# Optimization experiments

Hardware: AMD Instinct MI355X
Metric: run time of the kernel (lower is better)

The kernel has to match this reference:

```python
import jax, jax.numpy as jnp
import numpy as np

NU, NI, E = 200000, 100000, 500000
D, H, O = 128, 256, 128  # embedding_dim, hidden_dim, output_dim


def _sage(x_src, x_dst, src, dst, n_dst, W_l, b_l, W_r):
    """PyG SAGEConv (mean aggr): lin_l(mean_j x_src[j]) + lin_r(x_dst)."""
    msgs = x_src[src]                                            # [E, d_in]
    summed = jax.ops.segment_sum(msgs, dst, num_segments=n_dst)  # [n_dst, d_in]
    deg = jax.ops.segment_sum(jnp.ones(src.shape, x_src.dtype), dst, num_segments=n_dst)
    mean = summed / jnp.maximum(deg, 1.0)[:, None]
    return mean @ W_l + b_l + x_dst @ W_r


def setup_inputs() -> dict:
    key = jax.random.key(0)
    ks = jax.random.split(key, 18)

    def w(k, i, o):
        return jax.random.normal(k, (i, o), jnp.float32) / np.float32(np.sqrt(i))

    return {
        "x_user": jax.random.normal(ks[0], (NU, D), jnp.float32),
        "x_item": jax.random.normal(ks[1], (NI, D), jnp.float32),
        "edge_src": jax.random.randint(ks[2], (E,), 0, NU, jnp.int32),
        "edge_dst": jax.random.randint(ks[3], (E,), 0, NI, jnp.int32),
        # layer 1 (encoder): D -> H, one SAGEConv per edge type
        "W_l1_ui": w(ks[4], D, H), "W_r1_ui": w(ks[5], D, H), "b_l1_ui": jnp.zeros((H,), jnp.float32),
        "W_l1_iu": w(ks[6], D, H), "W_r1_iu": w(ks[7], D, H), "b_l1_iu": jnp.zeros((H,), jnp.float32),
        # layer 2 (projection): H -> O
        "W_l2_ui": w(ks[8], H, O), "W_r2_ui": w(ks[9], H, O), "b_l2_ui": jnp.zeros((O,), jnp.float32),
        "W_l2_iu": w(ks[10], H, O), "W_r2_iu": w(ks[11], H, O), "b_l2_iu": jnp.zeros((O,), jnp.float32),
    }


def reference(x_user, x_item, edge_src, edge_dst,
              W_l1_ui, W_r1_ui, b_l1_ui, W_l1_iu, W_r1_iu, b_l1_iu,
              W_l2_ui, W_r2_ui, b_l2_ui, W_l2_iu, W_r2_iu, b_l2_iu):
    # encoder layer: relu(SAGEConv) per destination node type (dropout=eval/no-op)
    h_item = jax.nn.relu(_sage(x_user, x_item, edge_src, edge_dst, NI, W_l1_ui, b_l1_ui, W_r1_ui))
    h_user = jax.nn.relu(_sage(x_item, x_user, edge_dst, edge_src, NU, W_l1_iu, b_l1_iu, W_r1_iu))
    # extra relu in RecommendationGNN.forward is a no-op after relu
    # projection layer: relu(SAGEConv), dropout=0
    o_item = jax.nn.relu(_sage(h_user, h_item, edge_src, edge_dst, NI, W_l2_ui, b_l2_ui, W_r2_ui))
    o_user = jax.nn.relu(_sage(h_item, h_user, edge_dst, edge_src, NU, W_l2_iu, b_l2_iu, W_r2_iu))
    return (o_user, o_item)
```

## Files before the change

kernel.cpp:

```cpp
#include <hip/hip_runtime.h>
#include <stdint.h>

typedef __attribute__((ext_vector_type(8))) short short8;
typedef __attribute__((ext_vector_type(4))) float f32x4;

#define SCAN_TILE 4096

__device__ __forceinline__ float bf2f(unsigned short u) {
  union { unsigned int i; float f; } v;
  v.i = ((unsigned int)u) << 16;
  return v.f;
}
__device__ __forceinline__ unsigned short f2bf(float f) {
  union { float f; unsigned int i; } v;
  v.f = f;
  unsigned int u = v.i;
  return (unsigned short)((u + 0x7FFFu + ((u >> 16) & 1u)) >> 16);
}
__device__ __forceinline__ unsigned int pack2(float a, float b) {
  return (unsigned int)f2bf(a) | ((unsigned int)f2bf(b) << 16);
}
__device__ __forceinline__ void add2(float& a, float& b, unsigned int v) {
  a += bf2f((unsigned short)(v & 0xffff));
  b += bf2f((unsigned short)(v >> 16));
}

__device__ __forceinline__ size_t fragS128(int row, int k) {
  return ((size_t)(row >> 4) * 4 + (size_t)(k >> 5)) * 512
       + (size_t)((((row & 15) + (((k >> 3) & 3) << 4)) << 3) + (k & 7));
}

__global__ __launch_bounds__(256) void build_wt_all(
    const float* __restrict__ Wl1ui, const float* __restrict__ Wr1ui,
    const float* __restrict__ Wl1iu, const float* __restrict__ Wr1iu,
    const float* __restrict__ Wl2ui, const float* __restrict__ Wr2ui,
    const float* __restrict__ Wl2iu, const float* __restrict__ Wr2iu,
    unsigned short* __restrict__ T1ui_l, unsigned short* __restrict__ T1ui_h,
    unsigned short* __restrict__ T1iu_l, unsigned short* __restrict__ T1iu_h,
    unsigned short* __restrict__ T2lui_l, unsigned short* __restrict__ T2lui_h,
    unsigned short* __restrict__ T2rui_l, unsigned short* __restrict__ T2rui_h,
    unsigned short* __restrict__ T2liu_l, unsigned short* __restrict__ T2liu_h,
    unsigned short* __restrict__ T2riu_l, unsigned short* __restrict__ T2riu_h)
{
  int idx = blockIdx.x * 256 + threadIdx.x;
  const float *W1, *W2;
  unsigned short *lo, *hi;
  int N, rel;
  if (idx < 65536)       { W1 = Wl1ui; W2 = Wr1ui;          lo = T1ui_l;  hi = T1ui_h;  N = 256; rel = idx; }
  else if (idx < 131072) { W1 = Wl1iu; W2 = Wr1iu;          lo = T1iu_l;  hi = T1iu_h;  N = 256; rel = idx - 65536; }
  else if (idx < 163840) { W1 = Wl2ui; W2 = Wl2ui + 128*128; lo = T2lui_l; hi = T2lui_h; N = 128; rel = idx - 131072; }
  else if (idx < 196608) { W1 = Wr2ui; W2 = Wr2ui + 128*128; lo = T2rui_l; hi = T2rui_h; N = 128; rel = idx - 163840; }
  else if (idx < 229376) { W1 = Wl2iu; W2 = Wl2iu + 128*128; lo = T2liu_l; hi = T2liu_h; N = 128; rel = idx - 196608; }
  else                   { W1 = Wr2iu; W2 = Wr2iu + 128*128; lo = T2riu_l; hi = T2riu_h; N = 128; rel = idx - 229376; }
  int n = rel >> 8;
  int k = rel & 255;
  float v = (k < 128) ? W1[(size_t)k * N + n] : W2[(size_t)(k - 128) * N + n];
  if (k < 128) lo[fragS128(n, k)] = f2bf(v);
  else         hi[fragS128(n, k - 128)] = f2bf(v);
}

__global__ __launch_bounds__(256) void conv_x(
    const float* __restrict__ xu, const float* __restrict__ xi,
    uint4* __restrict__ XfI, uint4* __restrict__ XfU,
    int NI, int NU, int MI, int MU)
{
  int u = blockIdx.x * 256 + threadIdx.x;
  int unitsI = MI * 16;
  const float* x; uint4* Xf; int M; int rel;
  if (u < unitsI) { x = xi; Xf = XfI; M = NI; rel = u; }
  else {
    rel = u - unitsI;
    if (rel >= MU * 16) return;
    x = xu; Xf = XfU; M = NU;
  }
  int c = rel >> 6;
  int s = rel & 63;
  int row = ((c >> 2) << 4) + (s & 15);
  int k = ((c & 3) << 5) + ((s >> 4) << 3);
  uint4 o = make_uint4(0u, 0u, 0u, 0u);
  if (row < M) {
    f32x4 a = *(const f32x4*)(x + (size_t)row * 128 + k);
    f32x4 b = *(const f32x4*)(x + (size_t)row * 128 + k + 4);
    o.x = pack2(a[0], a[1]); o.y = pack2(a[2], a[3]);
    o.z = pack2(b[0], b[1]); o.w = pack2(b[2], b[3]);
  }
  Xf[rel] = o;
}

__global__ __launch_bounds__(256) void hist(
    const int* __restrict__ esrc, const int* __restrict__ edst,
    int* __restrict__ cntAll, int NI, int E)
{
  int e = blockIdx.x * 256 + threadIdx.x;
  if (e >= E) return;
  atomicAdd(&cntAll[edst[e]], 1);
  atomicAdd(&cntAll[NI + esrc[e]], 1);
}

__global__ __launch_bounds__(256) void scan_p1(
    const int* __restrict__ cnt, int* __restrict__ tileSums, int NA)
{
  __shared__ int red[256];
  int b = blockIdx.x, t = threadIdx.x;
  int base = b * SCAN_TILE;
  int s = 0;
  for (int i = t; i < SCAN_TILE; i += 256) {
    int g = base + i;
    if (g < NA) s += cnt[g];
  }
  red[t] = s;
  __syncthreads();
  for (int d = 128; d > 0; d >>= 1) {
    if (t < d) red[t] += red[t + d];
    __syncthreads();
  }
  if (t == 0) tileSums[b] = red[0];
}

__global__ __launch_bounds__(256) void scan_p2(
    int* __restrict__ tileSums, int nTiles, int* __restrict__ offEnd)
{
  __shared__ int buf[256];
  int t = threadIdx.x;
  int v = (t < nTiles) ? tileSums[t] : 0;
  buf[t] = v;
  __syncthreads();
  for (int d = 1; d < 256; d <<= 1) {
    int x = (t >= d) ? buf[t - d] : 0;
    __syncthreads();
    buf[t] += x;
    __syncthreads();
  }
  if (t < nTiles) tileSums[t] = buf[t] - v;
  if (t == nTiles - 1) *offEnd = buf[t];
}

__global__ __launch_bounds__(256) void scan_p3(
    const int* __restrict__ cnt, const int* __restrict__ tileSums,
    int* __restrict__ off, int NA)
{
  __shared__ int red[256];
  int b = blockIdx.x, t = threadIdx.x;
  int base = b * SCAN_TILE + t * 16;
  int loc[16];
  int s = 0;
#pragma unroll
  for (int i = 0; i < 16; ++i) {
    int g = base + i;
    loc[i] = (g < NA) ? cnt[g] : 0;
    s += loc[i];
  }
  red[t] = s;
  __syncthreads();
  for (int d = 1; d < 256; d <<= 1) {
    int x = (t >= d) ? red[t - d] : 0;
    __syncthreads();
    red[t] += x;
    __syncthreads();
  }
  int run = tileSums[b] + red[t] - s;
#pragma unroll
  for (int i = 0; i < 16; ++i) {
    int g = base + i;
    if (g < NA) off[g] = run;
    run += loc[i];
  }
}

__global__ __launch_bounds__(256) void fill_idx(
    const int* __restrict__ esrc, const int* __restrict__ edst,
    const int* __restrict__ offAll, int* __restrict__ curAll,
    int* __restrict__ idxAll, int NI, int E)
{
  int e = blockIdx.x * 256 + threadIdx.x;
  if (e >= E) return;
  int s = esrc[e], d = edst[e];
  int pI = offAll[d] + atomicAdd(&curAll[d], 1);
  idxAll[pI] = s;
  int pU = offAll[NI + s] + atomicAdd(&curAll[NI + s], 1);
  idxAll[pU] = d;
}

__global__ __launch_bounds__(256) void build_mean(
    const float* __restrict__ xu, const float* __restrict__ xi,
    const int* __restrict__ idxAll, const int* __restrict__ offAll,
    unsigned short* __restrict__ MfI, unsigned short* __restrict__ MfU,
    int NI, int NA)
{
  int w2 = (blockIdx.x * 256 + threadIdx.x) >> 6;
  int l = threadIdx.x & 63;
  int h = l >> 5;
  int lh = l & 31;
  int node = w2 * 2 + h;
  if (node >= NA) return;
  bool isItem = (node < NI);
  const float* xo = isItem ? xu : xi;
  unsigned short* Mf = isItem ? MfI : MfU;
  int n = isItem ? node : (node - NI);
  int s = offAll[node], e = offAll[node + 1];

  f32x4 acc = (f32x4){0.f, 0.f, 0.f, 0.f};
  int j = s;
  for (; j + 1 < e; j += 2) {
    int g0 = idxAll[j];
    int g1 = idxAll[j + 1];
    f32x4 v0 = *(const f32x4*)(xo + (size_t)g0 * 128 + lh * 4);
    f32x4 v1 = *(const f32x4*)(xo + (size_t)g1 * 128 + lh * 4);
    acc += v0 + v1;
  }
  if (j < e) {
    int g = idxAll[j];
    acc += *(const f32x4*)(xo + (size_t)g * 128 + lh * 4);
  }

  float inv = 1.0f / (float)max(e - s, 1);
  uint2 o;
  o.x = pack2(acc[0] * inv, acc[1] * inv);
  o.y = pack2(acc[2] * inv, acc[3] * inv);
  *(uint2*)(Mf + fragS128(n, lh * 4)) = o;
}

__global__ __launch_bounds__(256) void seg_mean(
    const unsigned int* __restrict__ pU, const unsigned int* __restrict__ pI,
    const int* __restrict__ idxAll, const int* __restrict__ offAll,
    unsigned int* __restrict__ m2I, unsigned int* __restrict__ m2U,
    int NI, int NA)
{
  int w4 = (blockIdx.x * 256 + threadIdx.x) >> 6;
  int l = threadIdx.x & 63;
  int q = l >> 4;
  int lq = l & 15;
  int node = w4 * 4 + q;
  if (node >= NA) return;
  bool isItem = (node < NI);
  const unsigned int* p = isItem ? pU : pI;
  unsigned int* m2 = isItem ? m2I : m2U;
  int n = isItem ? node : (node - NI);
  int s = offAll[node], e = offAll[node + 1];

  float a0 = 0.f, a1 = 0.f, a2 = 0.f, a3 = 0.f,
        a4 = 0.f, a5 = 0.f, a6 = 0.f, a7 = 0.f;

  int j = s;
  for (; j + 1 < e; j += 2) {
    int g0 = idxAll[j];
    int g1 = idxAll[j + 1];
    uint4 v0 = *(const uint4*)(p + (size_t)g0 * 64 + lq * 4);
    uint4 v1 = *(const uint4*)(p + (size_t)g1 * 64 + lq * 4);
    add2(a0, a1, v0.x); add2(a2, a3, v0.y); add2(a4, a5, v0.z); add2(a6, a7, v0.w);
    add2(a0, a1, v1.x); add2(a2, a3, v1.y); add2(a4, a5, v1.z); add2(a6, a7, v1.w);
  }
  if (j < e) {
    int g = idxAll[j];
    uint4 v = *(const uint4*)(p + (size_t)g * 64 + lq * 4);
    add2(a0, a1, v.x); add2(a2, a3, v.y); add2(a4, a5, v.z); add2(a6, a7, v.w);
  }

  float inv = 1.0f / (float)max(e - s, 1);
  uint4 o;
  o.x = pack2(a0 * inv, a1 * inv);
  o.y = pack2(a2 * inv, a3 * inv);
  o.z = pack2(a4 * inv, a5 * inv);
  o.w = pack2(a6 * inv, a7 * inv);
  *(uint4*)(m2 + (size_t)n * 64 + lq * 4) = o;
}

__global__ __launch_bounds__(256, 3) void gemm_flat(
    const unsigned short* __restrict__ Alo, const unsigned short* __restrict__ Ahi,
    const unsigned short* __restrict__ Blo, const unsigned short* __restrict__ Bhi,
    const float* __restrict__ bias,
    const unsigned short* __restrict__ Madd,
    void* __restrict__ outp, unsigned short* __restrict__ outHi,
    int outF32, int outFrag, int M, int N, int doRelu)
{
  const int lane = threadIdx.x & 63;
  const int wave = threadIdx.x >> 6;
  const int m0 = blockIdx.x * 128 + (wave >> 1) * 64;
  const int n0 = blockIdx.y * 128 + (wave & 1) * 64;
  const int r16 = lane & 15;
  const int quad = lane >> 4;

  const uint4* AL = (const uint4*)Alo;
  const uint4* AH = (const uint4*)Ahi;
  const uint4* BL = (const uint4*)Blo;
  const uint4* BH = (const uint4*)Bhi;
  const size_t aB = (size_t)(m0 >> 4) * 256 + lane;
  const size_t bB = (size_t)(n0 >> 4) * 256 + lane;

  f32x4 acc[4][4];
#pragma unroll
  for (int i = 0; i < 4; ++i)
#pragma unroll
    for (int j = 0; j < 4; ++j) acc[i][j] = (f32x4){0.f, 0.f, 0.f, 0.f};

#pragma unroll
  for (int k0 = 0; k0 < 4; ++k0) {
    short8 av[4], bv[4];
#pragma unroll
    for (int g = 0; g < 4; ++g) {
      uint4 ta = AL[aB + (size_t)(g * 4 + k0) * 64];
      uint4 tb = BL[bB + (size_t)(g * 4 + k0) * 64];
      av[g] = *(const short8*)&ta;
      bv[g] = *(const short8*)&tb;
    }
#pragma unroll
    for (int mg = 0; mg < 4; ++mg)
#pragma unroll
      for (int ng = 0; ng < 4; ++ng)
        acc[mg][ng] = __builtin_amdgcn_mfma_f32_16x16x32_bf16(bv[ng], av[mg], acc[mg][ng], 0, 0, 0);
  }
#pragma unroll
  for (int k0 = 0; k0 < 4; ++k0) {
    short8 av[4], bv[4];
#pragma unroll
    for (int g = 0; g < 4; ++g) {
      uint4 ta = AH[aB + (size_t)(g * 4 + k0) * 64];
      uint4 tb = BH[bB + (size_t)(g * 4 + k0) * 64];
      av[g] = *(const short8*)&ta;
      bv[g] = *(const short8*)&tb;
    }
#pragma unroll
    for (int mg = 0; mg < 4; ++mg)
#pragma unroll
      for (int ng = 0; ng < 4; ++ng)
        acc[mg][ng] = __builtin_amdgcn_mfma_f32_16x16x32_bf16(bv[ng], av[mg], acc[mg][ng], 0, 0, 0);
  }

#pragma unroll
  for (int mg = 0; mg < 4; ++mg) {
    int row = m0 + mg * 16 + r16;
    if (row < M) {
#pragma unroll
      for (int ng = 0; ng < 4; ++ng) {
        int col = n0 + ng * 16 + quad * 4;
        f32x4 v = acc[mg][ng];
        if (bias) {
          f32x4 b4 = *(const f32x4*)(bias + col);
          v += b4;
        }
        if (Madd) {
          uint2 md = *(const uint2*)(Madd + (size_t)row * 128 + col);
          v[0] += bf2f((unsigned short)(md.x & 0xffff));
          v[1] += bf2f((unsigned short)(md.x >> 16));
          v[2] += bf2f((unsigned short)(md.y & 0xffff));
          v[3] += bf2f((unsigned short)(md.y >> 16));
        }
        if (doRelu) {
          v[0] = fmaxf(v[0], 0.0f); v[1] = fmaxf(v[1], 0.0f);
          v[2] = fmaxf(v[2], 0.0f); v[3] = fmaxf(v[3], 0.0f);
        }
        if (outF32) {
          *(f32x4*)((float*)outp + (size_t)row * N + col) = v;
        } else {
          uint2 o;
          o.x = pack2(v[0], v[1]);
          o.y = pack2(v[2], v[3]);
          if (outFrag) {
            if (col < 128) *(uint2*)((unsigned short*)outp + fragS128(row, col)) = o;
            else           *(uint2*)(outHi + fragS128(row, col - 128)) = o;
          } else {
            *(uint2*)((unsigned short*)outp + (size_t)row * N + col) = o;
          }
        }
      }
    }
  }
}

extern "C" void kernel_launch(void* const* d_in, const int* in_sizes, int n_in,
                              void* d_out, int out_size, void* d_ws, size_t ws_size,
                              hipStream_t stream)
{
  const float* x_user  = (const float*)d_in[0];
  const float* x_item  = (const float*)d_in[1];
  const int*   esrc    = (const int*)d_in[2];
  const int*   edst    = (const int*)d_in[3];
  const float* W_l1_ui = (const float*)d_in[4];
  const float* W_r1_ui = (const float*)d_in[5];
  const float* b_l1_ui = (const float*)d_in[6];
  const float* W_l1_iu = (const float*)d_in[7];
  const float* W_r1_iu = (const float*)d_in[8];
  const float* b_l1_iu = (const float*)d_in[9];
  const float* W_l2_ui = (const float*)d_in[10];
  const float* W_r2_ui = (const float*)d_in[11];
  const float* b_l2_ui = (const float*)d_in[12];
  const float* W_l2_iu = (const float*)d_in[13];
  const float* W_r2_iu = (const float*)d_in[14];
  const float* b_l2_iu = (const float*)d_in[15];

  const int NU = in_sizes[0] / 128;
  const int NI = in_sizes[1] / 128;
  const int E  = in_sizes[2];
  const int NA = NI + NU;
  const int MI = ((NI + 127) / 128) * 128;
  const int MU = ((NU + 127) / 128) * 128;

  char* ws = (char*)d_ws;
  size_t off = 0;
  auto alloc = [&](size_t bytes) -> void* {
    void* p = ws + off;
    off += (bytes + 255) & ~(size_t)255;
    return p;
  };

  int* cntAll = (int*)alloc((size_t)NA * 4);
  int* curAll = (int*)alloc((size_t)NA * 4);
  size_t zeroBytes = off;
  int* offAll   = (int*)alloc((size_t)(NA + 1) * 4);
  int* tileSums = (int*)alloc(256 * 4);
  int* idxAll   = (int*)alloc((size_t)2 * E * 4);
  unsigned short* T1ui_l  = (unsigned short*)alloc(256 * 128 * 2);
  unsigned short* T1ui_h  = (unsigned short*)alloc(256 * 128 * 2);
  unsigned short* T1iu_l  = (unsigned short*)alloc(256 * 128 * 2);
  unsigned short* T1iu_h  = (unsigned short*)alloc(256 * 128 * 2);
  unsigned short* T2lui_l = (unsigned short*)alloc(128 * 128 * 2);
  unsigned short* T2lui_h = (unsigned short*)alloc(128 * 128 * 2);
  unsigned short* T2rui_l = (unsigned short*)alloc(128 * 128 * 2);
  unsigned short* T2rui_h = (unsigned short*)alloc(128 * 128 * 2);
  unsigned short* T2liu_l = (unsigned short*)alloc(128 * 128 * 2);
  unsigned short* T2liu_h = (unsigned short*)alloc(128 * 128 * 2);
  unsigned short* T2riu_l = (unsigned short*)alloc(128 * 128 * 2);
  unsigned short* T2riu_h = (unsigned short*)alloc(128 * 128 * 2);
  unsigned short* h_item = (unsigned short*)alloc((size_t)MI * 256 * 2);
  unsigned short* h_item_hi = h_item + (size_t)MI * 128;
  unsigned short* h_user = (unsigned short*)alloc((size_t)MU * 256 * 2);
  unsigned short* h_user_hi = h_user + (size_t)MU * 128;
  char* R = (char*)alloc((size_t)(MI + MU) * 256 * 2);
  unsigned short* Mf_item = (unsigned short*)R;
  unsigned short* Mf_user = (unsigned short*)(R + (size_t)MI * 128 * 2);
  unsigned short* Xf_item = (unsigned short*)(R + (size_t)(MI + MU) * 128 * 2);
  unsigned short* Xf_user = (unsigned short*)(R + (size_t)(2 * MI + MU) * 128 * 2);
  unsigned short* p_user = (unsigned short*)R;
  unsigned short* p_item = (unsigned short*)(R + (size_t)NU * 128 * 2);
  unsigned short* m2I    = (unsigned short*)(R + (size_t)(NU + NI) * 128 * 2);
  unsigned short* m2U    = (unsigned short*)(R + (size_t)(NU + 2 * NI) * 128 * 2);

  float* out = (float*)d_out;

  hipMemsetAsync(ws, 0, zeroBytes, stream);

  build_wt_all<<<1024, 256, 0, stream>>>(
      W_l1_ui, W_r1_ui, W_l1_iu, W_r1_iu, W_l2_ui, W_r2_ui, W_l2_iu, W_r2_iu,
      T1ui_l, T1ui_h, T1iu_l, T1iu_h,
      T2lui_l, T2lui_h, T2rui_l, T2rui_h, T2liu_l, T2liu_h, T2riu_l, T2riu_h);

  int units = (MI + MU) * 16;
  conv_x<<<(units + 255) / 256, 256, 0, stream>>>(
      x_user, x_item, (uint4*)Xf_item, (uint4*)Xf_user, NI, NU, MI, MU);

  int egrid = (E + 255) / 256;
  int nTiles = (NA + SCAN_TILE - 1) / SCAN_TILE;
  hist<<<egrid, 256, 0, stream>>>(esrc, edst, cntAll, NI, E);
  scan_p1<<<nTiles, 256, 0, stream>>>(cntAll, tileSums, NA);
  scan_p2<<<1, 256, 0, stream>>>(tileSums, nTiles, offAll + NA);
  scan_p3<<<nTiles, 256, 0, stream>>>(cntAll, tileSums, offAll, NA);
  fill_idx<<<egrid, 256, 0, stream>>>(esrc, edst, offAll, curAll, idxAll, NI, E);

  int waves1 = (NA + 1) / 2;
  build_mean<<<(waves1 * 64 + 255) / 256, 256, 0, stream>>>(
      x_user, x_item, idxAll, offAll, Mf_item, Mf_user, NI, NA);

  dim3 gI(MI / 128, 2), gU(MU / 128, 2);
  gemm_flat<<<gI, 256, 0, stream>>>(Mf_item, Xf_item, T1ui_l, T1ui_h, b_l1_ui,
                                    nullptr, h_item, h_item_hi, 0, 1, NI, 256, 1);
  gemm_flat<<<gU, 256, 0, stream>>>(Mf_user, Xf_user, T1iu_l, T1iu_h, b_l1_iu,
                                    nullptr, h_user, h_user_hi, 0, 1, NU, 256, 1);

  dim3 pGu(MU / 128, 1), pGi(MI / 128, 1);
  gemm_flat<<<pGu, 256, 0, stream>>>(h_user, h_user_hi, T2lui_l, T2lui_h, nullptr,
                                     nullptr, p_user, nullptr, 0, 0, NU, 128, 0);
  gemm_flat<<<pGi, 256, 0, stream>>>(h_item, h_item_hi, T2liu_l, T2liu_h, nullptr,
                                     nullptr, p_item, nullptr, 0, 0, NI, 128, 0);

  int waves2 = (NA + 3) / 4;
  seg_mean<<<(waves2 * 64 + 255) / 256, 256, 0, stream>>>(
      (const unsigned int*)p_user, (const unsigned int*)p_item,
      idxAll, offAll, (unsigned int*)m2I, (unsigned int*)m2U, NI, NA);

  gemm_flat<<<pGi, 256, 0, stream>>>(h_item, h_item_hi, T2rui_l, T2rui_h, b_l2_ui,
                                     m2I, out + (size_t)NU * 128, nullptr, 1, 0, NI, 128, 1);
  gemm_flat<<<pGu, 256, 0, stream>>>(h_user, h_user_hi, T2riu_l, T2riu_h, b_l2_iu,
                                     m2U, out, nullptr, 1, 0, NU, 128, 1);
}
```

Baseline: 854.5 us.

## Stage B tiles in LDS and merge paired item/user GEMMs into one launch

The GEMM kernel now loads the 128-column B (weight) tile cooperatively into 32 KB of shared memory for each K-half, and the waves read B fragments from LDS instead of each wave fetching them from global memory. The first A fragment is prefetched before the barrier. Item and user GEMMs that share a shape are merged into a single launch through a parameter struct selected by block index, so six launches become three. Occupancy hint goes from 3 to 4 blocks. This adds barriers and LDS pressure, which may limit occupancy.

```diff
diff --git a/kernel.cpp b/kernel.cpp
--- a/kernel.cpp
+++ b/kernel.cpp
@@ -265,42 +265,70 @@
   *(uint4*)(m2 + (size_t)n * 64 + lq * 4) = o;
 }
 
-__global__ __launch_bounds__(256, 3) void gemm_flat(
-    const unsigned short* __restrict__ Alo, const unsigned short* __restrict__ Ahi,
-    const unsigned short* __restrict__ Blo, const unsigned short* __restrict__ Bhi,
-    const float* __restrict__ bias,
-    const unsigned short* __restrict__ Madd,
-    void* __restrict__ outp, unsigned short* __restrict__ outHi,
-    int outF32, int outFrag, int M, int N, int doRelu)
-{
-  const int lane = threadIdx.x & 63;
-  const int wave = threadIdx.x >> 6;
-  const int m0 = blockIdx.x * 128 + (wave >> 1) * 64;
-  const int n0 = blockIdx.y * 128 + (wave & 1) * 64;
+struct GemmP {
+  const unsigned short* Alo; const unsigned short* Ahi;
+  const unsigned short* Blo; const unsigned short* Bhi;
+  const float* bias;
+  const unsigned short* Madd;
+  void* outp; unsigned short* outHi;
+  int M;
+};
+
+__global__ __launch_bounds__(256, 4) void gemm_flat(
+    GemmP P0, GemmP P1, int rb0,
+    int outF32, int outFrag, int N, int doRelu)
+{
+  __shared__ uint4 lB[2048];
+
+  const int bx = blockIdx.x;
+  const bool first = (bx < rb0);
+  GemmP P = first ? P0 : P1;
+  const int mb = first ? bx : bx - rb0;
+
+  const int tid = threadIdx.x;
+  const int lane = tid & 63;
+  const int wave = tid >> 6;
+  const int m0 = mb * 128 + (wave >> 1) * 64;
+  const int nBase = blockIdx.y * 128;
+  const int n0 = nBase + (wave & 1) * 64;
   const int r16 = lane & 15;
   const int quad = lane >> 4;
-
-  const uint4* AL = (const uint4*)Alo;
-  const uint4* AH = (const uint4*)Ahi;
-  const uint4* BL = (const uint4*)Blo;
-  const uint4* BH = (const uint4*)Bhi;
+  const int cgl = (wave & 1) * 4;
+
+  const uint4* AL = (const uint4*)P.Alo;
+  const uint4* AH = (const uint4*)P.Ahi;
+  const uint4* BL = (const uint4*)P.Blo + (size_t)(nBase >> 4) * 256;
+  const uint4* BH = (const uint4*)P.Bhi + (size_t)(nBase >> 4) * 256;
   const size_t aB = (size_t)(m0 >> 4) * 256 + lane;
-  const size_t bB = (size_t)(n0 >> 4) * 256 + lane;
 
   f32x4 acc[4][4];
 #pragma unroll
   for (int i = 0; i < 4; ++i)
 #pragma unroll
     for (int j = 0; j < 4; ++j) acc[i][j] = (f32x4){0.f, 0.f, 0.f, 0.f};
+
+  short8 avp[4];
+#pragma unroll
+  for (int g = 0; g < 4; ++g) {
+    uint4 t = AL[aB + (size_t)(g * 4) * 64];
+    avp[g] = *(const short8*)&t;
+  }
+#pragma unroll
+  for (int i = 0; i < 8; ++i)
+    lB[i * 256 + tid] = BL[i * 256 + tid];
+  __syncthreads();
 
 #pragma unroll
   for (int k0 = 0; k0 < 4; ++k0) {
     short8 av[4], bv[4];
 #pragma unroll
     for (int g = 0; g < 4; ++g) {
-      uint4 ta = AL[aB + (size_t)(g * 4 + k0) * 64];
-      uint4 tb = BL[bB + (size_t)(g * 4 + k0) * 64];
-      av[g] = *(const short8*)&ta;
+      if (k0 == 0) av[g] = avp[g];
+      else {
+        uint4 t = AL[aB + (size_t)(g * 4 + k0) * 64];
+        av[g] = *(const short8*)&t;
+      }
+      uint4 tb = lB[((cgl + g) * 4 + k0) * 64 + lane];
       bv[g] = *(const short8*)&tb;
     }
 #pragma unroll
@@ -309,14 +337,29 @@
       for (int ng = 0; ng < 4; ++ng)
         acc[mg][ng] = __builtin_amdgcn_mfma_f32_16x16x32_bf16(bv[ng], av[mg], acc[mg][ng], 0, 0, 0);
   }
+  __syncthreads();
+
+#pragma unroll
+  for (int g = 0; g < 4; ++g) {
+    uint4 t = AH[aB + (size_t)(g * 4) * 64];
+    avp[g] = *(const short8*)&t;
+  }
+#pragma unroll
+  for (int i = 0; i < 8; ++i)
+    lB[i * 256 + tid] = BH[i * 256 + tid];
+  __syncthreads();
+
 #pragma unroll
   for (int k0 = 0; k0 < 4; ++k0) {
     short8 av[4], bv[4];
 #pragma unroll
     for (int g = 0; g < 4; ++g) {
-      uint4 ta = AH[aB + (size_t)(g * 4 + k0) * 64];
-      uint4 tb = BH[bB + (size_t)(g * 4 + k0) * 64];
-      av[g] = *(const short8*)&ta;
+      if (k0 == 0) av[g] = avp[g];
+      else {
+        uint4 t = AH[aB + (size_t)(g * 4 + k0) * 64];
+        av[g] = *(const short8*)&t;
+      }
+      uint4 tb = lB[((cgl + g) * 4 + k0) * 64 + lane];
       bv[g] = *(const short8*)&tb;
     }
 #pragma unroll
@@ -329,17 +372,17 @@
 #pragma unroll
   for (int mg = 0; mg < 4; ++mg) {
     int row = m0 + mg * 16 + r16;
-    if (row < M) {
+    if (row < P.M) {
 #pragma unroll
       for (int ng = 0; ng < 4; ++ng) {
         int col = n0 + ng * 16 + quad * 4;
         f32x4 v = acc[mg][ng];
-        if (bias) {
-          f32x4 b4 = *(const f32x4*)(bias + col);
+        if (P.bias) {
+          f32x4 b4 = *(const f32x4*)(P.bias + col);
           v += b4;
         }
-        if (Madd) {
-          uint2 md = *(const uint2*)(Madd + (size_t)row * 128 + col);
+        if (P.Madd) {
+          uint2 md = *(const uint2*)(P.Madd + (size_t)row * 128 + col);
           v[0] += bf2f((unsigned short)(md.x & 0xffff));
           v[1] += bf2f((unsigned short)(md.x >> 16));
           v[2] += bf2f((unsigned short)(md.y & 0xffff));
@@ -350,16 +393,16 @@
           v[2] = fmaxf(v[2], 0.0f); v[3] = fmaxf(v[3], 0.0f);
         }
         if (outF32) {
-          *(f32x4*)((float*)outp + (size_t)row * N + col) = v;
+          *(f32x4*)((float*)P.outp + (size_t)row * N + col) = v;
         } else {
           uint2 o;
           o.x = pack2(v[0], v[1]);
           o.y = pack2(v[2], v[3]);
           if (outFrag) {
-            if (col < 128) *(uint2*)((unsigned short*)outp + fragS128(row, col)) = o;
-            else           *(uint2*)(outHi + fragS128(row, col - 128)) = o;
+            if (col < 128) *(uint2*)((unsigned short*)P.outp + fragS128(row, col)) = o;
+            else           *(uint2*)(P.outHi + fragS128(row, col - 128)) = o;
           } else {
-            *(uint2*)((unsigned short*)outp + (size_t)row * N + col) = o;
+            *(uint2*)((unsigned short*)P.outp + (size_t)row * N + col) = o;
           }
         }
       }
@@ -460,25 +503,24 @@
   build_mean<<<(waves1 * 64 + 255) / 256, 256, 0, stream>>>(
       x_user, x_item, idxAll, offAll, Mf_item, Mf_user, NI, NA);
 
-  dim3 gI(MI / 128, 2), gU(MU / 128, 2);
-  gemm_flat<<<gI, 256, 0, stream>>>(Mf_item, Xf_item, T1ui_l, T1ui_h, b_l1_ui,
-                                    nullptr, h_item, h_item_hi, 0, 1, NI, 256, 1);
-  gemm_flat<<<gU, 256, 0, stream>>>(Mf_user, Xf_user, T1iu_l, T1iu_h, b_l1_iu,
-                                    nullptr, h_user, h_user_hi, 0, 1, NU, 256, 1);
-
-  dim3 pGu(MU / 128, 1), pGi(MI / 128, 1);
-  gemm_flat<<<pGu, 256, 0, stream>>>(h_user, h_user_hi, T2lui_l, T2lui_h, nullptr,
-                                     nullptr, p_user, nullptr, 0, 0, NU, 128, 0);
-  gemm_flat<<<pGi, 256, 0, stream>>>(h_item, h_item_hi, T2liu_l, T2liu_h, nullptr,
-                                     nullptr, p_item, nullptr, 0, 0, NI, 128, 0);
+  const int rbI = MI / 128, rbU = MU / 128;
+
+  GemmP l1i = {Mf_item, Xf_item, T1ui_l, T1ui_h, b_l1_ui, nullptr, h_item, h_item_hi, NI};
+  GemmP l1u = {Mf_user, Xf_user, T1iu_l, T1iu_h, b_l1_iu, nullptr, h_user, h_user_hi, NU};
+  gemm_flat<<<dim3(rbI + rbU, 2), 256, 0, stream>>>(l1i, l1u, rbI, 0, 1, 256, 1);
+
+  GemmP pi = {h_item, h_item_hi, T2liu_l, T2liu_h, nullptr, nullptr, p_item, nullptr, NI};
+  GemmP pu = {h_user, h_user_hi, T2lui_l, T2lui_h, nullptr, nullptr, p_user, nullptr, NU};
+  gemm_flat<<<dim3(rbI + rbU, 1), 256, 0, stream>>>(pi, pu, rbI, 0, 0, 128, 0);
 
   int waves2 = (NA + 3) / 4;
   seg_mean<<<(waves2 * 64 + 255) / 256, 256, 0, stream>>>(
       (const unsigned int*)p_user, (const unsigned int*)p_item,
       idxAll, offAll, (unsigned int*)m2I, (unsigned int*)m2U, NI, NA);
 
-  gemm_flat<<<pGi, 256, 0, stream>>>(h_item, h_item_hi, T2rui_l, T2rui_h, b_l2_ui,
-                                     m2I, out + (size_t)NU * 128, nullptr, 1, 0, NI, 128, 1);
-  gemm_flat<<<pGu, 256, 0, stream>>>(h_user, h_user_hi, T2riu_l, T2riu_h, b_l2_iu,
-                                     m2U, out, nullptr, 1, 0, NU, 128, 1);
-}
+  GemmP oi = {h_item, h_item_hi, T2rui_l, T2rui_h, b_l2_ui, m2I,
+              out + (size_t)NU * 128, nullptr, NI};
+  GemmP ou = {h_user, h_user_hi, T2riu_l, T2riu_h, b_l2_iu, m2U,
+              out, nullptr, NU};
+  gemm_flat<<<dim3(rbI + rbU, 1), 256, 0, stream>>>(oi, ou, rbI, 1, 0, 128, 1);
+}
```

Result: no change. 869.4 us (+1.7%).
